# Kernel optimization log

Measured on AMD Instinct MI355X. Metric: run time of the kernel, lower is better.

## Reference

```python
import jax, jax.numpy as jnp
import numpy as np
from jax import lax

B, C, H, W = 256, 768, 24, 24


def _corner_mask(h, w):
    # corners are never considered peaks in the original nested loops
    m = np.zeros((h, w), dtype=bool)
    m[[0, 0, -1, -1], [0, -1, 0, -1]] = True
    return jnp.asarray(m)


def get_peaks_pool(feat):
    # feat: [B, C, H, W]
    hm = jnp.mean(feat, axis=1)  # [B, H, W]
    # 3x3 local max/min with window clipped at the image border (SAME pad with
    # identity elements), exactly matching the original edge-case loops.
    mx = lax.reduce_window(hm, -jnp.inf, lax.max, (1, 3, 3), (1, 1, 1), 'SAME')
    mn = lax.reduce_window(hm, jnp.inf, lax.min, (1, 3, 3), (1, 1, 1), 'SAME')
    corner = _corner_mask(hm.shape[1], hm.shape[2])
    max_mask = ((hm >= mx) & ~corner).astype(feat.dtype)  # [B, H, W]
    min_mask = ((hm <= mn) & ~corner).astype(feat.dtype)
    # masked mean of feature vectors at peak locations
    f_max = jnp.einsum('bchw,bhw->bc', feat, max_mask) / jnp.sum(max_mask, axis=(1, 2))[:, None]
    f_min = jnp.einsum('bchw,bhw->bc', feat, min_mask) / jnp.sum(min_mask, axis=(1, 2))[:, None]
    f_gap = jnp.mean(feat, axis=(2, 3))  # global average pool
    return jnp.stack([f_max, f_min, f_gap], axis=2)  # [B, C, 3]


def _l2norm(x):
    return x / jnp.linalg.norm(x, axis=-1, keepdims=True)


def _cross_entropy(logits):
    # labels = arange(B): mean of -log_softmax diagonal
    logp = jax.nn.log_softmax(logits, axis=-1)
    return -jnp.mean(jnp.diagonal(logp))


def setup_inputs() -> dict:
    key = jax.random.key(0)
    k1, k2 = jax.random.split(key)
    return {
        'image_features1': jax.random.normal(k1, (B, C, H, W), dtype=jnp.float32),
        'image_features2': jax.random.normal(k2, (B, C, H, W), dtype=jnp.float32),
        'logit_scale': jnp.full((1,), 14.285, dtype=jnp.float32),
    }


def reference(image_features1, image_features2, logit_scale):
    p1 = get_peaks_pool(image_features1)  # [B, C, 3]
    p2 = get_peaks_pool(image_features2)
    e1 = _l2norm(jnp.concatenate([p1[:, :, 0], p1[:, :, 1], p1[:, :, 2]], axis=-1))  # [B, 3C]
    e2 = _l2norm(jnp.concatenate([p2[:, :, 0], p2[:, :, 1], p2[:, :, 2]], axis=-1))
    logits1 = logit_scale.reshape(()) * (e1 @ e2.T)  # [B, B]
    logits2 = logits1.T
    return (_cross_entropy(logits1) + _cross_entropy(logits2)) / 2
```

## Files before the change

kernel.cpp:

```cpp
#include <hip/hip_runtime.h>
#include <math.h>

#define BB   256
#define CC   768
#define HHX  24
#define WWX  24
#define HWX  576
#define HW4  144
#define EDIM 2304
#define NIMG 2

__global__ void k1_hm(const float* __restrict__ f1, const float* __restrict__ f2,
                      float* __restrict__ hm) {
    int blk = blockIdx.x;
    int img = blk >> 8;
    int b   = blk & 255;
    const float* base = ((img == 0) ? f1 : f2) + (size_t)b * CC * HWX;
    const float4* base4 = (const float4*)base;
    int t = threadIdx.x;
    int pos4 = t % HW4;
    int cg   = t / HW4;
    float4 acc = make_float4(0.f, 0.f, 0.f, 0.f);
    #pragma unroll 8
    for (int c = cg; c < CC; c += 4) {
        float4 v = base4[(size_t)c * HW4 + pos4];
        acc.x += v.x; acc.y += v.y; acc.z += v.z; acc.w += v.w;
    }
    __shared__ float4 part[HWX];
    part[t] = acc;
    __syncthreads();
    if (t < HW4) {
        float4 a = part[t], b4 = part[t + HW4], c4 = part[t + 2 * HW4], d4 = part[t + 3 * HW4];
        float4 s;
        s.x = a.x + b4.x + c4.x + d4.x;
        s.y = a.y + b4.y + c4.y + d4.y;
        s.z = a.z + b4.z + c4.z + d4.z;
        s.w = a.w + b4.w + c4.w + d4.w;
        ((float4*)(hm + (size_t)blk * HWX))[t] = s;
    }
}

__global__ void k3_sums(const float* __restrict__ f1, const float* __restrict__ f2,
                        const float* __restrict__ hm, float* __restrict__ cnt,
                        float* __restrict__ sums) {
    int blk = blockIdx.x;
    int img = blk >> 8, b = blk & 255;
    const float* base = ((img == 0) ? f1 : f2) + (size_t)b * CC * HWX;
    int t = threadIdx.x;
    int lane = t & 63;
    int wv   = t >> 6;

    __shared__ __align__(16) float sh[HWX];
    __shared__ __align__(16) float smm[HWX];
    __shared__ __align__(16) float smn[HWX];
    __shared__ int c0, c1;

    sh[t] = hm[(size_t)blk * HWX + t];
    if (t < HWX - 512) sh[512 + t] = hm[(size_t)blk * HWX + 512 + t];
    if (t == 0) { c0 = 0; c1 = 0; }
    __syncthreads();

    for (int p = t; p < HWX; p += 512) {
        int h = p / WWX, w = p % WWX;
        float v = sh[p];
        float mx = -__builtin_inff(), mn = __builtin_inff();
        #pragma unroll
        for (int dh = -1; dh <= 1; ++dh) {
            int hh = h + dh;
            if (hh < 0 || hh >= HHX) continue;
            #pragma unroll
            for (int dw = -1; dw <= 1; ++dw) {
                int ww = w + dw;
                if (ww < 0 || ww >= WWX) continue;
                float u = sh[hh * WWX + ww];
                mx = fmaxf(mx, u);
                mn = fminf(mn, u);
            }
        }
        bool corner = (p == 0) || (p == WWX - 1) || (p == (HHX - 1) * WWX) || (p == HWX - 1);
        bool ismax = (v >= mx) && !corner;
        bool ismin = (v <= mn) && !corner;
        smm[p] = ismax ? 1.f : 0.f;
        smn[p] = ismin ? 1.f : 0.f;
        if (ismax) atomicAdd(&c0, 1);
        if (ismin) atomicAdd(&c1, 1);
    }
    __syncthreads();
    if (t == 0) {
        cnt[blk * 2 + 0] = (float)c0;
        cnt[blk * 2 + 1] = (float)c1;
    }

    float4 ma0 = ((const float4*)smm)[lane];
    float4 ma1 = ((const float4*)smm)[64 + lane];
    float  ma2 = smm[512 + lane];
    float4 mi0 = ((const float4*)smn)[lane];
    float4 mi1 = ((const float4*)smn)[64 + lane];
    float  mi2 = smn[512 + lane];

    float* out = sums + (size_t)blk * EDIM;

    for (int c = wv; c < CC; c += 8) {
        const float4* p4 = (const float4*)(base + (size_t)c * HWX);
        float4 v0 = p4[lane];
        float4 v1 = p4[64 + lane];
        float  v2 = (base + (size_t)c * HWX)[512 + lane];

        float s0 = v0.x + v0.y + v0.z + v0.w + v1.x + v1.y + v1.z + v1.w + v2;
        float s1 = v0.x * ma0.x + v0.y * ma0.y + v0.z * ma0.z + v0.w * ma0.w;
        s1 = fmaf(v1.x, ma1.x, s1); s1 = fmaf(v1.y, ma1.y, s1);
        s1 = fmaf(v1.z, ma1.z, s1); s1 = fmaf(v1.w, ma1.w, s1);
        s1 = fmaf(v2, ma2, s1);
        float s2 = v0.x * mi0.x + v0.y * mi0.y + v0.z * mi0.z + v0.w * mi0.w;
        s2 = fmaf(v1.x, mi1.x, s2); s2 = fmaf(v1.y, mi1.y, s2);
        s2 = fmaf(v1.z, mi1.z, s2); s2 = fmaf(v1.w, mi1.w, s2);
        s2 = fmaf(v2, mi2, s2);

        #pragma unroll
        for (int off = 32; off; off >>= 1) {
            s0 += __shfl_down(s0, off, 64);
            s1 += __shfl_down(s1, off, 64);
            s2 += __shfl_down(s2, off, 64);
        }
        if (lane == 0) {
            out[c]          = s1;
            out[CC + c]     = s2;
            out[2 * CC + c] = s0;
        }
    }
}

__global__ void k4_norm(float* __restrict__ sums, const float* __restrict__ cnt,
                        float* __restrict__ e2t) {
    int blk = blockIdx.x;
    int img = blk >> 8, b = blk & 255;
    int t = threadIdx.x;
    float invmax = 1.f / cnt[blk * 2 + 0];
    float invmin = 1.f / cnt[blk * 2 + 1];
    const float invgap = 1.f / (float)HWX;
    float* e = sums + (size_t)blk * EDIM;

    float val[9];
    float sq = 0.f;
    #pragma unroll
    for (int j = 0; j < 9; ++j) {
        int k = t + 256 * j;
        float d = (k < CC) ? invmax : (k < 2 * CC) ? invmin : invgap;
        float v = e[k] * d;
        val[j] = v;
        sq = fmaf(v, v, sq);
    }
    __shared__ float red[256];
    red[t] = sq;
    __syncthreads();
    for (int s = 128; s; s >>= 1) {
        if (t < s) red[t] += red[t + s];
        __syncthreads();
    }
    float rn = 1.f / sqrtf(red[0]);
    #pragma unroll
    for (int j = 0; j < 9; ++j) {
        int k = t + 256 * j;
        float v = val[j] * rn;
        e[k] = v;
        if (img == 1) e2t[(size_t)k * BB + b] = v;
    }
}

__global__ void k5_logits(const float* __restrict__ e, const float* __restrict__ e2t,
                          const float* __restrict__ scale_p, float* __restrict__ logits,
                          float* __restrict__ logitsT) {
    int blk = blockIdx.x;
    int j = threadIdx.x;
    __shared__ float s1[2][EDIM];
    for (int r = 0; r < 2; ++r)
        for (int k = j; k < EDIM; k += 256)
            s1[r][k] = e[(size_t)(2 * blk + r) * EDIM + k];
    __syncthreads();
    float scale = scale_p[0];
    float a0 = 0.f, a1 = 0.f;
    for (int k = 0; k < EDIM; k += 4) {
        float b0 = e2t[(size_t)(k + 0) * BB + j];
        float b1 = e2t[(size_t)(k + 1) * BB + j];
        float b2 = e2t[(size_t)(k + 2) * BB + j];
        float b3 = e2t[(size_t)(k + 3) * BB + j];
        a0 = fmaf(s1[0][k + 0], b0, a0); a1 = fmaf(s1[1][k + 0], b0, a1);
        a0 = fmaf(s1[0][k + 1], b1, a0); a1 = fmaf(s1[1][k + 1], b1, a1);
        a0 = fmaf(s1[0][k + 2], b2, a0); a1 = fmaf(s1[1][k + 2], b2, a1);
        a0 = fmaf(s1[0][k + 3], b3, a0); a1 = fmaf(s1[1][k + 3], b3, a1);
    }
    float r0 = scale * a0, r1 = scale * a1;
    logits[(size_t)(2 * blk + 0) * BB + j] = r0;
    logits[(size_t)(2 * blk + 1) * BB + j] = r1;
    logitsT[(size_t)j * BB + (2 * blk + 0)] = r0;
    logitsT[(size_t)j * BB + (2 * blk + 1)] = r1;
}

__global__ void k6_lse(const float* __restrict__ logits, const float* __restrict__ logitsT,
                       float* __restrict__ lse) {
    int g = blockIdx.x * 4 + (threadIdx.x >> 6);
    int lane = threadIdx.x & 63;
    const float* row = (g < BB) ? (logits + (size_t)g * BB)
                                : (logitsT + (size_t)(g - BB) * BB);
    float4 v = ((const float4*)row)[lane];
    float m = fmaxf(fmaxf(v.x, v.y), fmaxf(v.z, v.w));
    #pragma unroll
    for (int off = 32; off; off >>= 1) m = fmaxf(m, __shfl_xor(m, off, 64));
    float s = expf(v.x - m) + expf(v.y - m) + expf(v.z - m) + expf(v.w - m);
    #pragma unroll
    for (int off = 32; off; off >>= 1) s += __shfl_xor(s, off, 64);
    if (lane == 0) lse[g] = m + logf(s);
}

__global__ void k7_loss(const float* __restrict__ logits, const float* __restrict__ lse,
                        float* __restrict__ out) {
    int i = threadIdx.x;
    float v = 0.5f * (lse[i] + lse[BB + i]) - logits[(size_t)i * BB + i];
    __shared__ float red[256];
    red[i] = v;
    __syncthreads();
    for (int s = 128; s; s >>= 1) {
        if (i < s) red[i] += red[i + s];
        __syncthreads();
    }
    if (i == 0) out[0] = red[0] * (1.f / (float)BB);
}

extern "C" void kernel_launch(void* const* d_in, const int* in_sizes, int n_in,
                              void* d_out, int out_size, void* d_ws, size_t ws_size,
                              hipStream_t stream) {
    const float* f1 = (const float*)d_in[0];
    const float* f2 = (const float*)d_in[1];
    const float* scale_p = (const float*)d_in[2];
    float* out = (float*)d_out;

    float* ws = (float*)d_ws;
    const size_t off_hm      = 0;
    const size_t off_cnt     = off_hm      + (size_t)NIMG * BB * HWX;
    const size_t off_sums    = off_cnt     + (size_t)NIMG * BB * 2;
    const size_t off_e2t     = off_sums    + (size_t)NIMG * BB * EDIM;
    const size_t off_logits  = off_e2t     + (size_t)EDIM * BB;
    const size_t off_logitsT = off_logits  + (size_t)BB * BB;
    const size_t off_lse     = off_logitsT + (size_t)BB * BB;

    float* hm      = ws + off_hm;
    float* cnt     = ws + off_cnt;
    float* sums    = ws + off_sums;
    float* e2t     = ws + off_e2t;
    float* logits  = ws + off_logits;
    float* logitsT = ws + off_logitsT;
    float* lse     = ws + off_lse;

    hipLaunchKernelGGL(k1_hm,     dim3(NIMG * BB), dim3(HWX), 0, stream, f1, f2, hm);
    hipLaunchKernelGGL(k3_sums,   dim3(NIMG * BB), dim3(512), 0, stream, f1, f2, hm, cnt, sums);
    hipLaunchKernelGGL(k4_norm,   dim3(NIMG * BB), dim3(256), 0, stream, sums, cnt, e2t);
    hipLaunchKernelGGL(k5_logits, dim3(128),       dim3(256), 0, stream, sums, e2t, scale_p, logits, logitsT);
    hipLaunchKernelGGL(k6_lse,    dim3(128),       dim3(256), 0, stream, logits, logitsT, lse);
    hipLaunchKernelGGL(k7_loss,   dim3(1),         dim3(256), 0, stream, logits, lse, out);
}
```

Baseline: 1.094 ms.

## Fuse normalization into sums kernel and split-K the logits GEMM

```diff
diff --git a/kernel.cpp b/kernel.cpp
--- a/kernel.cpp
+++ b/kernel.cpp
@@ -41,8 +41,8 @@
 }
 
 __global__ void k3_sums(const float* __restrict__ f1, const float* __restrict__ f2,
-                        const float* __restrict__ hm, float* __restrict__ cnt,
-                        float* __restrict__ sums) {
+                        const float* __restrict__ hm, float* __restrict__ e,
+                        float* __restrict__ e2t) {
     int blk = blockIdx.x;
     int img = blk >> 8, b = blk & 255;
     const float* base = ((img == 0) ? f1 : f2) + (size_t)b * CC * HWX;
@@ -53,6 +53,7 @@
     __shared__ __align__(16) float sh[HWX];
     __shared__ __align__(16) float smm[HWX];
     __shared__ __align__(16) float smn[HWX];
+    __shared__ __align__(16) float esum[EDIM];
     __shared__ int c0, c1;
 
     sh[t] = hm[(size_t)blk * HWX + t];
@@ -86,10 +87,6 @@
         if (ismin) atomicAdd(&c1, 1);
     }
     __syncthreads();
-    if (t == 0) {
-        cnt[blk * 2 + 0] = (float)c0;
-        cnt[blk * 2 + 1] = (float)c1;
-    }
 
     float4 ma0 = ((const float4*)smm)[lane];
     float4 ma1 = ((const float4*)smm)[64 + lane];
@@ -97,8 +94,6 @@
     float4 mi0 = ((const float4*)smn)[lane];
     float4 mi1 = ((const float4*)smn)[64 + lane];
     float  mi2 = smn[512 + lane];
-
-    float* out = sums + (size_t)blk * EDIM;
 
     for (int c = wv; c < CC; c += 8) {
         const float4* p4 = (const float4*)(base + (size_t)c * HWX);
@@ -123,77 +118,95 @@
             s2 += __shfl_down(s2, off, 64);
         }
         if (lane == 0) {
-            out[c]          = s1;
-            out[CC + c]     = s2;
-            out[2 * CC + c] = s0;
+            esum[c]          = s1;
+            esum[CC + c]     = s2;
+            esum[2 * CC + c] = s0;
         }
     }
-}
-
-__global__ void k4_norm(float* __restrict__ sums, const float* __restrict__ cnt,
-                        float* __restrict__ e2t) {
-    int blk = blockIdx.x;
-    int img = blk >> 8, b = blk & 255;
+    __syncthreads();
+
+    float invmax = 1.f / (float)c0;
+    float invmin = 1.f / (float)c1;
+    const float invgap = 1.f / (float)HWX;
+
+    float val[5];
+    float sq = 0.f;
+    #pragma unroll
+    for (int jj = 0; jj < 4; ++jj) {
+        int k = t + 512 * jj;
+        float d = (k < CC) ? invmax : (k < 2 * CC) ? invmin : invgap;
+        float v = esum[k] * d;
+        val[jj] = v;
+        sq = fmaf(v, v, sq);
+    }
+    if (t < 256) {
+        int k = 2048 + t;
+        float v = esum[k] * invgap;
+        val[4] = v;
+        sq = fmaf(v, v, sq);
+    } else {
+        val[4] = 0.f;
+    }
+
+    smm[t] = sq;
+    __syncthreads();
+    for (int s = 256; s; s >>= 1) {
+        if (t < s) smm[t] += smm[t + s];
+        __syncthreads();
+    }
+    float rn = 1.f / sqrtf(smm[0]);
+
+    float* eo = e + (size_t)blk * EDIM;
+    #pragma unroll
+    for (int jj = 0; jj < 4; ++jj) {
+        int k = t + 512 * jj;
+        float v = val[jj] * rn;
+        eo[k] = v;
+        if (img == 1) e2t[(size_t)k * BB + b] = v;
+    }
+    if (t < 256) {
+        int k = 2048 + t;
+        float v = val[4] * rn;
+        eo[k] = v;
+        if (img == 1) e2t[(size_t)k * BB + b] = v;
+    }
+}
+
+__global__ void __launch_bounds__(1024)
+k5_logits(const float* __restrict__ e, const float* __restrict__ e2t,
+          const float* __restrict__ scale_p, float* __restrict__ logits,
+          float* __restrict__ logitsT) {
+    int i = blockIdx.x;
     int t = threadIdx.x;
-    float invmax = 1.f / cnt[blk * 2 + 0];
-    float invmin = 1.f / cnt[blk * 2 + 1];
-    const float invgap = 1.f / (float)HWX;
-    float* e = sums + (size_t)blk * EDIM;
-
-    float val[9];
-    float sq = 0.f;
-    #pragma unroll
-    for (int j = 0; j < 9; ++j) {
-        int k = t + 256 * j;
-        float d = (k < CC) ? invmax : (k < 2 * CC) ? invmin : invgap;
-        float v = e[k] * d;
-        val[j] = v;
-        sq = fmaf(v, v, sq);
-    }
-    __shared__ float red[256];
-    red[t] = sq;
-    __syncthreads();
-    for (int s = 128; s; s >>= 1) {
-        if (t < s) red[t] += red[t + s];
-        __syncthreads();
-    }
-    float rn = 1.f / sqrtf(red[0]);
-    #pragma unroll
-    for (int j = 0; j < 9; ++j) {
-        int k = t + 256 * j;
-        float v = val[j] * rn;
-        e[k] = v;
-        if (img == 1) e2t[(size_t)k * BB + b] = v;
-    }
-}
-
-__global__ void k5_logits(const float* __restrict__ e, const float* __restrict__ e2t,
-                          const float* __restrict__ scale_p, float* __restrict__ logits,
-                          float* __restrict__ logitsT) {
-    int blk = blockIdx.x;
-    int j = threadIdx.x;
-    __shared__ float s1[2][EDIM];
-    for (int r = 0; r < 2; ++r)
-        for (int k = j; k < EDIM; k += 256)
-            s1[r][k] = e[(size_t)(2 * blk + r) * EDIM + k];
-    __syncthreads();
-    float scale = scale_p[0];
-    float a0 = 0.f, a1 = 0.f;
-    for (int k = 0; k < EDIM; k += 4) {
+    int j = t & 255;
+    int h = t >> 8;
+    __shared__ float s1row[EDIM];
+    __shared__ float part[4][256];
+    for (int k = t; k < EDIM; k += 1024)
+        s1row[k] = e[(size_t)i * EDIM + k];
+    __syncthreads();
+
+    float acc = 0.f;
+    int k0 = h * (EDIM / 4);
+    #pragma unroll 4
+    for (int kk = 0; kk < EDIM / 4; kk += 4) {
+        int k = k0 + kk;
         float b0 = e2t[(size_t)(k + 0) * BB + j];
         float b1 = e2t[(size_t)(k + 1) * BB + j];
         float b2 = e2t[(size_t)(k + 2) * BB + j];
         float b3 = e2t[(size_t)(k + 3) * BB + j];
-        a0 = fmaf(s1[0][k + 0], b0, a0); a1 = fmaf(s1[1][k + 0], b0, a1);
-        a0 = fmaf(s1[0][k + 1], b1, a0); a1 = fmaf(s1[1][k + 1], b1, a1);
-        a0 = fmaf(s1[0][k + 2], b2, a0); a1 = fmaf(s1[1][k + 2], b2, a1);
-        a0 = fmaf(s1[0][k + 3], b3, a0); a1 = fmaf(s1[1][k + 3], b3, a1);
-    }
-    float r0 = scale * a0, r1 = scale * a1;
-    logits[(size_t)(2 * blk + 0) * BB + j] = r0;
-    logits[(size_t)(2 * blk + 1) * BB + j] = r1;
-    logitsT[(size_t)j * BB + (2 * blk + 0)] = r0;
-    logitsT[(size_t)j * BB + (2 * blk + 1)] = r1;
+        acc = fmaf(s1row[k + 0], b0, acc);
+        acc = fmaf(s1row[k + 1], b1, acc);
+        acc = fmaf(s1row[k + 2], b2, acc);
+        acc = fmaf(s1row[k + 3], b3, acc);
+    }
+    part[h][j] = acc;
+    __syncthreads();
+    if (h == 0) {
+        float r = scale_p[0] * (part[0][j] + part[1][j] + part[2][j] + part[3][j]);
+        logits[(size_t)i * BB + j] = r;
+        logitsT[(size_t)j * BB + i] = r;
+    }
 }
 
 __global__ void k6_lse(const float* __restrict__ logits, const float* __restrict__ logitsT,
@@ -236,25 +249,22 @@
 
     float* ws = (float*)d_ws;
     const size_t off_hm      = 0;
-    const size_t off_cnt     = off_hm      + (size_t)NIMG * BB * HWX;
-    const size_t off_sums    = off_cnt     + (size_t)NIMG * BB * 2;
+    const size_t off_sums    = off_hm      + (size_t)NIMG * BB * HWX;
     const size_t off_e2t     = off_sums    + (size_t)NIMG * BB * EDIM;
     const size_t off_logits  = off_e2t     + (size_t)EDIM * BB;
     const size_t off_logitsT = off_logits  + (size_t)BB * BB;
     const size_t off_lse     = off_logitsT + (size_t)BB * BB;
 
     float* hm      = ws + off_hm;
-    float* cnt     = ws + off_cnt;
     float* sums    = ws + off_sums;
     float* e2t     = ws + off_e2t;
     float* logits  = ws + off_logits;
     float* logitsT = ws + off_logitsT;
     float* lse     = ws + off_lse;
 
-    hipLaunchKernelGGL(k1_hm,     dim3(NIMG * BB), dim3(HWX), 0, stream, f1, f2, hm);
-    hipLaunchKernelGGL(k3_sums,   dim3(NIMG * BB), dim3(512), 0, stream, f1, f2, hm, cnt, sums);
-    hipLaunchKernelGGL(k4_norm,   dim3(NIMG * BB), dim3(256), 0, stream, sums, cnt, e2t);
-    hipLaunchKernelGGL(k5_logits, dim3(128),       dim3(256), 0, stream, sums, e2t, scale_p, logits, logitsT);
-    hipLaunchKernelGGL(k6_lse,    dim3(128),       dim3(256), 0, stream, logits, logitsT, lse);
-    hipLaunchKernelGGL(k7_loss,   dim3(1),         dim3(256), 0, stream, logits, lse, out);
-}
+    hipLaunchKernelGGL(k1_hm,     dim3(NIMG * BB), dim3(HWX),  0, stream, f1, f2, hm);
+    hipLaunchKernelGGL(k3_sums,   dim3(NIMG * BB), dim3(512),  0, stream, f1, f2, hm, sums, e2t);
+    hipLaunchKernelGGL(k5_logits, dim3(BB),        dim3(1024), 0, stream, sums, e2t, scale_p, logits, logitsT);
+    hipLaunchKernelGGL(k6_lse,    dim3(128),       dim3(256),  0, stream, logits, logitsT, lse);
+    hipLaunchKernelGGL(k7_loss,   dim3(1),         dim3(256),  0, stream, logits, lse, out);
+}
```

After: 1.012 ms. 7.6% less time.
